# Kernel optimization log

Hardware: AMD Instinct MI355X
Metric: run time of the kernel (lower is better)

Reference implementation:

```python
import jax, jax.numpy as jnp
import numpy as np

K = 4096
D = 128
B = 8
T = 3000
EMA_DECAY = 0.99
EMA_EPS = 1e-05
DEAD_THRESHOLD = 2.0


def setup_inputs() -> dict:
    key = jax.random.key(0)
    k1, k2, k3 = jax.random.split(key, 3)
    z = jax.random.normal(k1, (B, D, T), dtype=jnp.float32)
    codebook = jax.random.normal(k2, (K, D), dtype=jnp.float32) * 0.05  # pretrained-like
    ema_cluster_size = jnp.ones((K,), dtype=jnp.float32)
    ema_embed_avg = codebook.copy()
    return {"z": z, "codebook": codebook,
            "ema_cluster_size": ema_cluster_size, "ema_embed_avg": ema_embed_avg}


def reference(z, codebook, ema_cluster_size, ema_embed_avg):
    b, d, t = z.shape
    z_t = jnp.transpose(z, (0, 2, 1))            # [B, T, D]
    z_flat = z_t.reshape(-1, d)                  # [N, D]

    x2 = jnp.sum(z_flat * z_flat, axis=1, keepdims=True)
    y2 = jnp.sum(codebook * codebook, axis=1)[None, :]
    distances = x2 + y2 - 2.0 * (z_flat @ codebook.T)
    indices = jnp.argmin(distances, axis=1)      # [N]

    q = codebook[indices].reshape(b, t, d)       # [B, T, D]
    loss_commit = jnp.mean((z_t - jax.lax.stop_gradient(q)) ** 2)

    # --- EMA update (torch: @torch.no_grad, training mode) ---
    zf = jax.lax.stop_gradient(z_flat)
    counts = jax.ops.segment_sum(jnp.ones_like(indices, dtype=jnp.float32), indices, num_segments=K)
    embed_sum = jax.ops.segment_sum(zf, indices, num_segments=K)   # [K, D]
    new_cs = ema_cluster_size * EMA_DECAY + counts * (1.0 - EMA_DECAY)
    new_ea = ema_embed_avg * EMA_DECAY + embed_sum * (1.0 - EMA_DECAY)
    n = jnp.sum(new_cs)
    cluster_size = (new_cs + EMA_EPS) / (n + K * EMA_EPS) * n
    embed = new_ea / jnp.clip(cluster_size, 1e-12)[:, None]

    # dead-code reset: resample dead entries from the batch
    dead = new_cs < DEAD_THRESHOLD                                 # [K] bool
    rand_idx = jax.random.randint(jax.random.key(42), (K,), 0, zf.shape[0])
    sampled = zf[rand_idx]                                          # [K, D]
    new_codebook = jnp.where(dead[:, None], sampled, embed)
    new_cs = jnp.where(dead, 1.0, new_cs)
    new_ea = jnp.where(dead[:, None], sampled, new_ea)

    # straight-through estimator
    q_ste = z_t + jax.lax.stop_gradient(q - z_t)
    z_q = jnp.transpose(q_ste, (0, 2, 1))        # [B, D, T]
    codes = indices.reshape(b, t)[None, :, None, :]  # [1, B, 1, T]

    return (z_q, codes, loss_commit, new_codebook, new_cs, new_ea)
```

## Files before the change

kernel.cpp:

```cpp
#include <hip/hip_runtime.h>
#include <stdint.h>

#define KCB 4096
#define DIM 128
#define BSZ 8
#define TLEN 3000
#define NPT 24000
#define KD (KCB*DIM)
#define BDT (BSZ*DIM*TLEN)

#define OFF_ZQ    0
#define OFF_CODES 3072000
#define OFF_LOSS  3096000
#define OFF_CB    3096001
#define OFF_CS    3620289
#define OFF_EA    3624385

#define OUT_ZH    0
#define OUT_ZL    1536000
#define OUT_CBH   3096004
#define OUT_CBL   3358148

#define WS_LOSS   0
#define WS_NTOT   1
#define WS_COUNTS 16
#define WS_Y2     (WS_COUNTS + 4096)
#define WS_X2     (WS_Y2 + 4096)
#define WS_CS0    (WS_X2 + 24000)
#define WS_RAND   (WS_CS0 + 4096)
#define WS_IDX    (WS_RAND + 4096)
#define WS_RCNT   (WS_IDX + 24000)
#define WS_RLIST  (WS_RCNT + 16)
#define RCAP      8192

#define EPS_CAND 2e-3f
#define CAND_MAX 8

typedef __attribute__((ext_vector_type(8))) short bf16x8;
typedef __attribute__((ext_vector_type(4))) float f32x4;
typedef __attribute__((ext_vector_type(4))) int i32x4;

__device__ __forceinline__ unsigned short f2bf(float f) {
  uint32_t u = __float_as_uint(f);
  uint32_t r = (u + 0x7FFFu + ((u >> 16) & 1u)) >> 16;
  return (unsigned short)r;
}
__device__ __forceinline__ float bf2f(unsigned short h) {
  return __uint_as_float(((uint32_t)h) << 16);
}

__device__ __forceinline__ void async16(const void* g, void* l) {
  __builtin_amdgcn_global_load_lds(
      (const __attribute__((address_space(1))) void*)g,
      (__attribute__((address_space(3))) void*)l, 16, 0, 0);
}

__device__ __forceinline__ void threefry2x32(uint32_t k0, uint32_t k1,
                                             uint32_t x0, uint32_t x1,
                                             uint32_t& o0, uint32_t& o1) {
  const uint32_t ks0 = k0, ks1 = k1, ks2 = k0 ^ k1 ^ 0x1BD11BDAu;
  const int r0[4] = {13, 15, 26, 6};
  const int r1[4] = {17, 29, 16, 24};
  x0 += ks0; x1 += ks1;
  #pragma unroll
  for (int i = 0; i < 5; ++i) {
    #pragma unroll
    for (int j = 0; j < 4; ++j) {
      int r = (i & 1) ? r1[j] : r0[j];
      x0 += x1;
      x1 = (x1 << r) | (x1 >> (32 - r));
      x1 ^= x0;
    }
    uint32_t ia = (uint32_t)((i + 1) % 3), ib = (uint32_t)((i + 2) % 3);
    uint32_t a = (ia == 0) ? ks0 : (ia == 1) ? ks1 : ks2;
    uint32_t b = (ib == 0) ? ks0 : (ib == 1) ? ks1 : ks2;
    x0 += a;
    x1 += b + (uint32_t)(i + 1);
  }
  o0 = x0; o1 = x1;
}

__device__ __forceinline__ float np_sumsq_128(const float* __restrict__ v) {
  float r[8];
  #pragma unroll
  for (int j = 0; j < 8; ++j) r[j] = __fmul_rn(v[j], v[j]);
  #pragma unroll
  for (int i = 8; i < DIM; i += 8) {
    #pragma unroll
    for (int j = 0; j < 8; ++j)
      r[j] = __fadd_rn(r[j], __fmul_rn(v[i + j], v[i + j]));
  }
  return __fadd_rn(__fadd_rn(__fadd_rn(r[0], r[1]), __fadd_rn(r[2], r[3])),
                   __fadd_rn(__fadd_rn(r[4], r[5]), __fadd_rn(r[6], r[7])));
}

__global__ void prep_z_kernel(const float* __restrict__ z,
                              unsigned short* __restrict__ zh,
                              unsigned short* __restrict__ zl,
                              float* __restrict__ x2) {
  __shared__ float zt[64 * 132];
  const int tid = threadIdx.x;
  const int n0 = blockIdx.x * 64;
  {
    int nl = tid & 63, dd = tid >> 6;
    int n = n0 + nl;
    int b = n / TLEN, t = n - b * TLEN;
    const float* zbase = z + (size_t)b * (DIM * TLEN) + t;
    #pragma unroll
    for (int d = dd; d < DIM; d += 4) zt[nl * 132 + d] = zbase[(size_t)d * TLEN];
  }
  __syncthreads();
  if (tid < 64) x2[n0 + tid] = np_sumsq_128(zt + tid * 132);

  int r = tid >> 2, d0 = (tid & 3) * 32;
  const float* src = zt + r * 132 + d0;
  size_t base = (size_t)(n0 + r) * 128 + d0;
  #pragma unroll
  for (int c = 0; c < 4; ++c) {
    i32x4 wh, wl;
    #pragma unroll
    for (int q = 0; q < 4; ++q) {
      float f0 = -2.0f * src[c * 8 + q * 2], f1 = -2.0f * src[c * 8 + q * 2 + 1];
      unsigned short h0 = f2bf(f0), h1 = f2bf(f1);
      unsigned short l0 = f2bf(f0 - bf2f(h0)), l1 = f2bf(f1 - bf2f(h1));
      wh[q] = (int)((uint32_t)h0 | ((uint32_t)h1 << 16));
      wl[q] = (int)((uint32_t)l0 | ((uint32_t)l1 << 16));
    }
    *(i32x4*)(zh + base + c * 8) = wh;
    *(i32x4*)(zl + base + c * 8) = wl;
  }
}

__global__ void prep_cb_kernel(const float* __restrict__ cb,
                               unsigned short* __restrict__ cbh,
                               unsigned short* __restrict__ cbl,
                               float* __restrict__ y2) {
  int k = blockIdx.x * 256 + threadIdx.x;
  const float4* row4 = (const float4*)(cb + (size_t)k * DIM);
  float racc[8];
  #pragma unroll
  for (int j = 0; j < 8; ++j) racc[j] = 0.f;
  #pragma unroll 4
  for (int c2 = 0; c2 < 16; ++c2) {
    float4 a = row4[c2 * 2], b = row4[c2 * 2 + 1];
    float f[8] = {a.x, a.y, a.z, a.w, b.x, b.y, b.z, b.w};
    i32x4 wh, wl;
    #pragma unroll
    for (int q = 0; q < 4; ++q) {
      float f0 = f[q * 2], f1 = f[q * 2 + 1];
      unsigned short h0 = f2bf(f0), h1 = f2bf(f1);
      unsigned short l0 = f2bf(f0 - bf2f(h0)), l1 = f2bf(f1 - bf2f(h1));
      wh[q] = (int)((uint32_t)h0 | ((uint32_t)h1 << 16));
      wl[q] = (int)((uint32_t)l0 | ((uint32_t)l1 << 16));
    }
    int cs = c2 ^ (k & 7);
    *(i32x4*)(cbh + (size_t)k * DIM + cs * 8) = wh;
    *(i32x4*)(cbl + (size_t)k * DIM + cs * 8) = wl;
    #pragma unroll
    for (int j = 0; j < 8; ++j)
      racc[j] = __fadd_rn(racc[j], __fmul_rn(f[j], f[j]));
  }
  y2[k] = __fadd_rn(__fadd_rn(__fadd_rn(racc[0], racc[1]), __fadd_rn(racc[2], racc[3])),
                    __fadd_rn(__fadd_rn(racc[4], racc[5]), __fadd_rn(racc[6], racc[7])));
}

__global__ void ea_init_kernel(const float* __restrict__ ema_ea, float* __restrict__ out_ea) {
  int i = blockIdx.x * 256 + threadIdx.x;
  out_ea[i] = 0.99f * ema_ea[i];
}

__launch_bounds__(256)
__global__ void mfma_argmin_kernel(const unsigned short* __restrict__ zh,
                                   const unsigned short* __restrict__ zl,
                                   const unsigned short* __restrict__ cbh,
                                   const unsigned short* __restrict__ cbl,
                                   const float* __restrict__ y2g,
                                   const float* __restrict__ x2g,
                                   const float* __restrict__ z,
                                   const float* __restrict__ cb,
                                   int* __restrict__ idx_out,
                                   float* __restrict__ codes_out,
                                   int* __restrict__ rcnt,
                                   int* __restrict__ rlist) {
  __shared__ alignas(16) unsigned short zh_t[64 * 128];
  __shared__ alignas(16) unsigned short zl_t[64 * 128];
  __shared__ alignas(16) unsigned short Ah_t[64 * 128];
  __shared__ alignas(16) unsigned short Al_t[64 * 128];
  __shared__ float tv[64 * 24];
  __shared__ int   ti[64 * 24];

  const int tid = threadIdx.x;
  const int wv = tid >> 6, lane = tid & 63;
  const int kw = wv & 1, nw = wv >> 1;
  const int lg = lane >> 4, lc = lane & 15;
  const int n0 = blockIdx.x * 64;

  {
    const char* gh = (const char*)cbh + (size_t)(wv * 4) * 1024 + lane * 16;
    const char* gl_ = (const char*)cbl + (size_t)(wv * 4) * 1024 + lane * 16;
    char* lh = (char*)Ah_t + wv * 4096;
    char* ll = (char*)Al_t + wv * 4096;
    #pragma unroll
    for (int i = 0; i < 4; ++i) {
      async16(gh + i * 1024, lh + i * 1024);
      async16(gl_ + i * 1024, ll + i * 1024);
    }
  }

  {
    int r = tid >> 2, c0 = (tid & 3) * 4;
    const i32x4* gzh = (const i32x4*)(zh + (size_t)(n0 + r) * 128);
    const i32x4* gzl = (const i32x4*)(zl + (size_t)(n0 + r) * 128);
    #pragma unroll
    for (int c = 0; c < 4; ++c) {
      int cc = (c0 + c) ^ (r & 7);
      ((i32x4*)zh_t)[r * 16 + cc] = gzh[c0 + c];
      ((i32x4*)zl_t)[r * 16 + cc] = gzl[c0 + c];
    }
  }

  float t1v[2], t2v[2], t3v[2];
  int   t1i[2], t2i[2], t3i[2];
  #pragma unroll
  for (int ns = 0; ns < 2; ++ns) {
    t1v[ns] = t2v[ns] = t3v[ns] = 3.402823466e+38f;
    t1i[ns] = t2i[ns] = t3i[ns] = 0x7FFFFFFF;
  }

  const int arow0 = kw * 32 + lc,  arow1 = kw * 32 + 16 + lc;
  const int zrow0 = nw * 32 + lc,  zrow1 = nw * 32 + 16 + lc;

  for (int tile = 0; tile < 64; ++tile) {
    asm volatile("s_waitcnt vmcnt(0)" ::: "memory");
    __syncthreads();

    const int kb = tile * 64 + kw * 32;
    float4 y40 = *(const float4*)(y2g + kb + lg * 4);
    float4 y41 = *(const float4*)(y2g + kb + 16 + lg * 4);
    f32x4 acc[2][2];
    #pragma unroll
    for (int ns = 0; ns < 2; ++ns) {
      acc[0][ns][0] = y40.x; acc[0][ns][1] = y40.y; acc[0][ns][2] = y40.z; acc[0][ns][3] = y40.w;
      acc[1][ns][0] = y41.x; acc[1][ns][1] = y41.y; acc[1][ns][2] = y41.z; acc[1][ns][3] = y41.w;
    }

    #pragma unroll
    for (int ds = 0; ds < 4; ++ds) {
      int cA0 = (ds * 4 + lg) ^ (arow0 & 7);
      int cA1 = (ds * 4 + lg) ^ (arow1 & 7);
      bf16x8 a0h = *(const bf16x8*)&Ah_t[arow0 * 128 + cA0 * 8];
      bf16x8 a0l = *(const bf16x8*)&Al_t[arow0 * 128 + cA0 * 8];
      bf16x8 a1h = *(const bf16x8*)&Ah_t[arow1 * 128 + cA1 * 8];
      bf16x8 a1l = *(const bf16x8*)&Al_t[arow1 * 128 + cA1 * 8];
      int cz0 = (ds * 4 + lg) ^ (zrow0 & 7);
      int cz1 = (ds * 4 + lg) ^ (zrow1 & 7);
      bf16x8 z0h = *(const bf16x8*)&zh_t[zrow0 * 128 + cz0 * 8];
      bf16x8 z0l = *(const bf16x8*)&zl_t[zrow0 * 128 + cz0 * 8];
      bf16x8 z1h = *(const bf16x8*)&zh_t[zrow1 * 128 + cz1 * 8];
      bf16x8 z1l = *(const bf16x8*)&zl_t[zrow1 * 128 + cz1 * 8];
      acc[0][0] = __builtin_amdgcn_mfma_f32_16x16x32_bf16(a0h, z0h, acc[0][0], 0, 0, 0);
      acc[0][0] = __builtin_amdgcn_mfma_f32_16x16x32_bf16(a0h, z0l, acc[0][0], 0, 0, 0);
      acc[0][0] = __builtin_amdgcn_mfma_f32_16x16x32_bf16(a0l, z0h, acc[0][0], 0, 0, 0);
      acc[0][1] = __builtin_amdgcn_mfma_f32_16x16x32_bf16(a0h, z1h, acc[0][1], 0, 0, 0);
      acc[0][1] = __builtin_amdgcn_mfma_f32_16x16x32_bf16(a0h, z1l, acc[0][1], 0, 0, 0);
      acc[0][1] = __builtin_amdgcn_mfma_f32_16x16x32_bf16(a0l, z1h, acc[0][1], 0, 0, 0);
      acc[1][0] = __builtin_amdgcn_mfma_f32_16x16x32_bf16(a1h, z0h, acc[1][0], 0, 0, 0);
      acc[1][0] = __builtin_amdgcn_mfma_f32_16x16x32_bf16(a1h, z0l, acc[1][0], 0, 0, 0);
      acc[1][0] = __builtin_amdgcn_mfma_f32_16x16x32_bf16(a1l, z0h, acc[1][0], 0, 0, 0);
      acc[1][1] = __builtin_amdgcn_mfma_f32_16x16x32_bf16(a1h, z1h, acc[1][1], 0, 0, 0);
      acc[1][1] = __builtin_amdgcn_mfma_f32_16x16x32_bf16(a1h, z1l, acc[1][1], 0, 0, 0);
      acc[1][1] = __builtin_amdgcn_mfma_f32_16x16x32_bf16(a1l, z1h, acc[1][1], 0, 0, 0);
    }

    __syncthreads();

    if (tile + 1 < 64) {
      const char* gh = (const char*)cbh + (size_t)(tile + 1) * 16384 + (size_t)(wv * 4) * 1024 + lane * 16;
      const char* gl_ = (const char*)cbl + (size_t)(tile + 1) * 16384 + (size_t)(wv * 4) * 1024 + lane * 16;
      char* lh = (char*)Ah_t + wv * 4096;
      char* ll = (char*)Al_t + wv * 4096;
      #pragma unroll
      for (int i = 0; i < 4; ++i) {
        async16(gh + i * 1024, lh + i * 1024);
        async16(gl_ + i * 1024, ll + i * 1024);
      }
    }

    #pragma unroll
    for (int ks = 0; ks < 2; ++ks) {
      int kbase = kb + ks * 16 + lg * 4;
      #pragma unroll
      for (int ns = 0; ns < 2; ++ns) {
        float fm = fminf(fminf(acc[ks][ns][0], acc[ks][ns][1]),
                         fminf(acc[ks][ns][2], acc[ks][ns][3]));
        if (fm < t3v[ns]) {
          #pragma unroll
          for (int q = 0; q < 4; ++q) {
            float v = acc[ks][ns][q];
            int kidx = kbase + q;
            bool c1 = v < t1v[ns], c2 = v < t2v[ns], c3 = v < t3v[ns];
            float n3v = c2 ? t2v[ns] : (c3 ? v : t3v[ns]);
            int   n3i = c2 ? t2i[ns] : (c3 ? kidx : t3i[ns]);
            float n2v = c1 ? t1v[ns] : (c2 ? v : t2v[ns]);
            int   n2i = c1 ? t1i[ns] : (c2 ? kidx : t2i[ns]);
            t1v[ns] = c1 ? v : t1v[ns]; t1i[ns] = c1 ? kidx : t1i[ns];
            t2v[ns] = n2v; t2i[ns] = n2i;
            t3v[ns] = n3v; t3i[ns] = n3i;
          }
        }
      }
    }
  }

  #pragma unroll
  for (int ns = 0; ns < 2; ++ns) {
    int row = nw * 32 + ns * 16 + lc;
    int base = row * 24 + (kw * 4 + lg) * 3;
    tv[base + 0] = t1v[ns]; ti[base + 0] = t1i[ns];
    tv[base + 1] = t2v[ns]; ti[base + 1] = t2i[ns];
    tv[base + 2] = t3v[ns]; ti[base + 2] = t3i[ns];
  }
  __syncthreads();

  if (tid < 64) {
    int n = n0 + tid;
    float bv = 3.402823466e+38f; int bi = 0x7FFFFFFF;
    for (int e = 0; e < 24; ++e) {
      float v = tv[tid * 24 + e]; int i2 = ti[tid * 24 + e];
      if (v < bv || (v == bv && i2 < bi)) { bv = v; bi = i2; }
    }
    int ci[CAND_MAX]; int cnt = 0;
    float lim = bv + EPS_CAND;
    for (int e = 0; e < 24; ++e) {
      float v = tv[tid * 24 + e];
      if (v <= lim && cnt < CAND_MAX) {
        int x = ti[tid * 24 + e];
        int p = cnt++;
        while (p > 0 && ci[p - 1] > x) { ci[p] = ci[p - 1]; --p; }
        ci[p] = x;
      }
    }
    if (cnt == 1) {
      idx_out[n] = ci[0];
      codes_out[n] = (float)ci[0];
    } else {
      int slot = atomicAdd(rcnt, 1);
      if (slot < RCAP) {
        int* e = rlist + slot * 10;
        e[0] = n; e[1] = cnt;
        for (int c = 0; c < CAND_MAX; ++c) e[2 + c] = (c < cnt) ? ci[c] : 0;
        idx_out[n] = ci[0];
        codes_out[n] = (float)ci[0];
      } else {
        int b = n / TLEN, t = n - b * TLEN;
        const float* zr = z + (size_t)b * (DIM * TLEN) + t;
        float bestv = 0.f; int kbest = ci[0];
        for (int c = 0; c < cnt; ++c) {
          int k = ci[c];
          const float* cr = cb + (size_t)k * DIM;
          float dot = 0.f;
          for (int d = 0; d < DIM; ++d)
            dot = __fmaf_rn(zr[(size_t)d * TLEN], cr[d], dot);
          float tt = __fadd_rn(x2g[n], y2g[k]);
          float dist = __fsub_rn(tt, __fmul_rn(2.0f, dot));
          if (c == 0 || dist < bestv) { bestv = dist; kbest = k; }
        }
        idx_out[n] = kbest;
        codes_out[n] = (float)kbest;
      }
    }
  }
}

__global__ void rescore_kernel(const float* __restrict__ z, const float* __restrict__ cb,
                               const float* __restrict__ x2g, const float* __restrict__ y2g,
                               const int* __restrict__ rcnt, const int* __restrict__ rlist,
                               int* __restrict__ idx_out, float* __restrict__ codes_out) {
  int w = (blockIdx.x * 256 + threadIdx.x) >> 6;
  int lane = threadIdx.x & 63;
  int nw = (gridDim.x * 256) >> 6;
  int total = *rcnt; if (total > RCAP) total = RCAP;
  for (int i = w; i < total; i += nw) {
    const int* e = rlist + i * 10;
    int n = e[0], cnt = e[1];
    int b = n / TLEN, t = n - b * TLEN;
    const float* zr = z + (size_t)b * (DIM * TLEN) + t;
    float dist = 3.402823466e+38f;
    int k = e[2 + (lane < cnt ? lane : 0)];
    if (lane < cnt) {
      const float* cr = cb + (size_t)k * DIM;
      float dot = 0.f;
      #pragma unroll 8
      for (int d = 0; d < DIM; ++d)
        dot = __fmaf_rn(zr[(size_t)d * TLEN], cr[d], dot);
      float tt = __fadd_rn(x2g[n], y2g[k]);
      dist = __fsub_rn(tt, __fmul_rn(2.0f, dot));
    }
    float bestv = 0.f; int kbest = 0;
    for (int c = 0; c < cnt; ++c) {
      float v = __shfl(dist, c);
      int kk = __shfl(k, c);
      if (c == 0 || v < bestv) { bestv = v; kbest = kk; }
    }
    if (lane == 0) {
      idx_out[n] = kbest;
      codes_out[n] = (float)kbest;
    }
  }
}

__global__ void ea_scatter_kernel(const unsigned short* __restrict__ zh,
                                  const unsigned short* __restrict__ zl,
                                  const int* __restrict__ idx,
                                  float* __restrict__ ea_out,
                                  float* __restrict__ counts) {
  int n = (blockIdx.x * 256 + threadIdx.x) >> 6;
  int lane = threadIdx.x & 63;
  int k = idx[n];
  uint32_t h = *(const uint32_t*)(zh + (size_t)n * 128 + lane * 2);
  uint32_t l = *(const uint32_t*)(zl + (size_t)n * 128 + lane * 2);
  float f0 = bf2f((unsigned short)(h & 0xffffu)) + bf2f((unsigned short)(l & 0xffffu));
  float f1 = bf2f((unsigned short)(h >> 16)) + bf2f((unsigned short)(l >> 16));
  float* dst = ea_out + (size_t)k * DIM + lane * 2;
  atomicAdd(dst, -0.005f * f0);
  atomicAdd(dst + 1, -0.005f * f1);
  if (lane == 0) atomicAdd(counts + k, 1.0f);
}

__global__ void zq_loss_kernel(const float* __restrict__ z, const float* __restrict__ cb,
                               const int* __restrict__ idx,
                               float* __restrict__ zq_out, float* __restrict__ loss_ws) {
  __shared__ float qt[64 * 132];
  const int tid = threadIdx.x;
  const int n0 = blockIdx.x * 64;
  {
    int r = tid >> 2, c = tid & 3;
    int k = idx[n0 + r];
    const float4* src = (const float4*)(cb + (size_t)k * DIM) + c * 8;
    float4* dst = (float4*)(qt + r * 132) + c * 8;
    #pragma unroll
    for (int j = 0; j < 8; ++j) dst[j] = src[j];
  }
  __syncthreads();
  int nl = tid & 63, dd = tid >> 6;
  int n = n0 + nl;
  int b = n / TLEN, t = n - b * TLEN;
  float* zqb = zq_out + (size_t)b * (DIM * TLEN) + t;
  const float* zb = z + (size_t)b * (DIM * TLEN) + t;
  float sq = 0.f;
  #pragma unroll
  for (int d = dd; d < DIM; d += 4) {
    float q = qt[nl * 132 + d];
    zqb[(size_t)d * TLEN] = q;
    float diff = zb[(size_t)d * TLEN] - q;
    sq = fmaf(diff, diff, sq);
  }
  #pragma unroll
  for (int m = 1; m <= 32; m <<= 1) sq += __shfl_xor(sq, m);
  __shared__ float ps[4];
  if ((tid & 63) == 0) ps[tid >> 6] = sq;
  __syncthreads();
  if (tid == 0) atomicAdd(loss_ws, ps[0] + ps[1] + ps[2] + ps[3]);
}

__global__ void cs_rand_kernel(const float* __restrict__ ema_cs, const float* __restrict__ counts,
                               float* __restrict__ cs0, uint32_t* __restrict__ rnd,
                               float* __restrict__ ntot) {
  int k = blockIdx.x * 256 + threadIdx.x;
  float v = 0.99f * ema_cs[k] + 0.01f * counts[k];
  cs0[k] = v;

  uint32_t o0, o1;
  threefry2x32(0u, 42u, 0u, (uint32_t)k, o0, o1);
  uint32_t bits = o0 ^ o1;
  uint32_t hi = bits >> 16, lo = bits & 0xffffu;
  const uint32_t span = 24000u, mult = 23296u;
  uint32_t off = ((hi % span) * mult + (lo % span)) % span;
  rnd[k] = off;

  float s = v;
  #pragma unroll
  for (int m = 1; m <= 32; m <<= 1) s += __shfl_xor(s, m);
  __shared__ float ps[4];
  if ((threadIdx.x & 63) == 0) ps[threadIdx.x >> 6] = s;
  __syncthreads();
  if (threadIdx.x == 0) atomicAdd(ntot, ps[0] + ps[1] + ps[2] + ps[3]);
}

__global__ void finalize_kernel(const float* __restrict__ z, const float* __restrict__ cs0_ws,
                                const uint32_t* __restrict__ rnd,
                                const float* __restrict__ ntot_ws, const float* __restrict__ loss_ws,
                                float* __restrict__ out) {
  int i = blockIdx.x * 256 + threadIdx.x;
  int k = i >> 7, d = i & (DIM - 1);
  float cs0 = cs0_ws[k];
  float ntot = *ntot_ws;
  float* ea = out + OFF_EA;
  float ea0 = ea[i];
  float csz = (cs0 + 1e-5f) / (ntot + (float)KCB * 1e-5f) * ntot;
  float embed = ea0 / fmaxf(csz, 1e-12f);
  bool dead = cs0 < 2.0f;
  uint32_t rn = rnd[k];
  int bb = (int)(rn / TLEN), tt = (int)(rn % TLEN);
  float sampled = z[(size_t)bb * (DIM * TLEN) + (size_t)d * TLEN + tt];
  out[OFF_CB + i] = dead ? sampled : embed;
  ea[i] = dead ? sampled : ea0;
  if (d == 0) out[OFF_CS + k] = dead ? 1.0f : cs0;
  if (i == 0) out[OFF_LOSS] = (*loss_ws) * (1.0f / (float)BDT);
}

extern "C" void kernel_launch(void* const* d_in, const int* in_sizes, int n_in,
                              void* d_out, int out_size, void* d_ws, size_t ws_size,
                              hipStream_t stream) {
  const float* z      = (const float*)d_in[0];
  const float* cb     = (const float*)d_in[1];
  const float* ema_cs = (const float*)d_in[2];
  const float* ema_ea = (const float*)d_in[3];
  float* out = (float*)d_out;
  float* wsf = (float*)d_ws;

  unsigned short* zh  = (unsigned short*)(out + OUT_ZH);
  unsigned short* zl  = (unsigned short*)(out + OUT_ZL);
  unsigned short* cbh = (unsigned short*)(out + OUT_CBH);
  unsigned short* cbl = (unsigned short*)(out + OUT_CBL);

  hipMemsetAsync(d_ws, 0, (size_t)(16 + 4096) * sizeof(float), stream);
  hipMemsetAsync(wsf + WS_RCNT, 0, 16 * sizeof(float), stream);

  prep_cb_kernel<<<KCB / 256, 256, 0, stream>>>(cb, cbh, cbl, wsf + WS_Y2);
  prep_z_kernel<<<NPT / 64, 256, 0, stream>>>(z, zh, zl, wsf + WS_X2);
  ea_init_kernel<<<KD / 256, 256, 0, stream>>>(ema_ea, out + OFF_EA);

  mfma_argmin_kernel<<<NPT / 64, 256, 0, stream>>>(zh, zl, cbh, cbl,
                                                   wsf + WS_Y2, wsf + WS_X2,
                                                   z, cb,
                                                   (int*)(wsf + WS_IDX), out + OFF_CODES,
                                                   (int*)(wsf + WS_RCNT), (int*)(wsf + WS_RLIST));
  rescore_kernel<<<64, 256, 0, stream>>>(z, cb, wsf + WS_X2, wsf + WS_Y2,
                                         (const int*)(wsf + WS_RCNT), (const int*)(wsf + WS_RLIST),
                                         (int*)(wsf + WS_IDX), out + OFF_CODES);

  ea_scatter_kernel<<<NPT * 64 / 256, 256, 0, stream>>>(zh, zl, (int*)(wsf + WS_IDX),
                                                        out + OFF_EA, wsf + WS_COUNTS);
  zq_loss_kernel<<<NPT / 64, 256, 0, stream>>>(z, cb, (int*)(wsf + WS_IDX),
                                               out + OFF_ZQ, wsf + WS_LOSS);
  cs_rand_kernel<<<KCB / 256, 256, 0, stream>>>(ema_cs, wsf + WS_COUNTS,
                                                wsf + WS_CS0, (uint32_t*)(wsf + WS_RAND),
                                                wsf + WS_NTOT);
  finalize_kernel<<<KD / 256, 256, 0, stream>>>(z, wsf + WS_CS0, (uint32_t*)(wsf + WS_RAND),
                                                wsf + WS_NTOT, wsf + WS_LOSS, out);
}
```

Before: 236.1 us.

## Split codebook search across two block columns with merge kernel

The argmin kernel now splits the codebook into two halves along a second grid dimension. Each block has 128 threads and computes partial best values and indices for 64 points over 2048 codes. Near-ties inside a block are resolved in-kernel with exact FP32 dot products. A new merge kernel picks the winner per point and sends cross-half near-ties to the existing rescore list. This doubles the block count and shrinks shared memory per block to raise occupancy and parallelism, at the cost of an extra kernel launch, partial-result traffic and z tiles loaded twice.

```diff
diff --git a/kernel.cpp b/kernel.cpp
--- a/kernel.cpp
+++ b/kernel.cpp
@@ -32,6 +32,8 @@
 #define WS_RCNT   (WS_IDX + 24000)
 #define WS_RLIST  (WS_RCNT + 16)
 #define RCAP      8192
+#define WS_PBV    (WS_RLIST + RCAP*10)
+#define WS_PBK    (WS_PBV + 2*NPT)
 
 #define EPS_CAND 2e-3f
 #define CAND_MAX 8
@@ -92,6 +94,16 @@
   }
   return __fadd_rn(__fadd_rn(__fadd_rn(r[0], r[1]), __fadd_rn(r[2], r[3])),
                    __fadd_rn(__fadd_rn(r[4], r[5]), __fadd_rn(r[6], r[7])));
+}
+
+__device__ __forceinline__ float np_exact_dist(const float* __restrict__ zr,
+                                               const float* __restrict__ cr,
+                                               float x2v, float y2v) {
+  float dot = 0.f;
+  for (int d = 0; d < DIM; ++d)
+    dot = __fmaf_rn(zr[(size_t)d * TLEN], cr[d], dot);
+  float tt = __fadd_rn(x2v, y2v);
+  return __fsub_rn(tt, __fmul_rn(2.0f, dot));
 }
 
 __global__ void prep_z_kernel(const float* __restrict__ z,
@@ -169,7 +181,7 @@
   out_ea[i] = 0.99f * ema_ea[i];
 }
 
-__launch_bounds__(256)
+__launch_bounds__(128)
 __global__ void mfma_argmin_kernel(const unsigned short* __restrict__ zh,
                                    const unsigned short* __restrict__ zl,
                                    const unsigned short* __restrict__ cbh,
@@ -178,26 +190,24 @@
                                    const float* __restrict__ x2g,
                                    const float* __restrict__ z,
                                    const float* __restrict__ cb,
-                                   int* __restrict__ idx_out,
-                                   float* __restrict__ codes_out,
-                                   int* __restrict__ rcnt,
-                                   int* __restrict__ rlist) {
+                                   float* __restrict__ pbv,
+                                   int* __restrict__ pbk) {
   __shared__ alignas(16) unsigned short zh_t[64 * 128];
   __shared__ alignas(16) unsigned short zl_t[64 * 128];
-  __shared__ alignas(16) unsigned short Ah_t[64 * 128];
-  __shared__ alignas(16) unsigned short Al_t[64 * 128];
-  __shared__ float tv[64 * 24];
-  __shared__ int   ti[64 * 24];
+  __shared__ alignas(16) unsigned short Ah_t[32 * 128];
+  __shared__ alignas(16) unsigned short Al_t[32 * 128];
 
   const int tid = threadIdx.x;
   const int wv = tid >> 6, lane = tid & 63;
-  const int kw = wv & 1, nw = wv >> 1;
+  const int nw = wv;
   const int lg = lane >> 4, lc = lane & 15;
   const int n0 = blockIdx.x * 64;
+  const int hy = blockIdx.y;
+  const size_t kofs = (size_t)hy * 2048;
 
   {
-    const char* gh = (const char*)cbh + (size_t)(wv * 4) * 1024 + lane * 16;
-    const char* gl_ = (const char*)cbl + (size_t)(wv * 4) * 1024 + lane * 16;
+    const char* gh = (const char*)cbh + kofs * 256 + (size_t)wv * 4096 + lane * 16;
+    const char* gl_ = (const char*)cbl + kofs * 256 + (size_t)wv * 4096 + lane * 16;
     char* lh = (char*)Ah_t + wv * 4096;
     char* ll = (char*)Al_t + wv * 4096;
     #pragma unroll
@@ -208,11 +218,11 @@
   }
 
   {
-    int r = tid >> 2, c0 = (tid & 3) * 4;
+    int r = tid >> 1, c0 = (tid & 1) * 8;
     const i32x4* gzh = (const i32x4*)(zh + (size_t)(n0 + r) * 128);
     const i32x4* gzl = (const i32x4*)(zl + (size_t)(n0 + r) * 128);
     #pragma unroll
-    for (int c = 0; c < 4; ++c) {
+    for (int c = 0; c < 8; ++c) {
       int cc = (c0 + c) ^ (r & 7);
       ((i32x4*)zh_t)[r * 16 + cc] = gzh[c0 + c];
       ((i32x4*)zl_t)[r * 16 + cc] = gzl[c0 + c];
@@ -227,14 +237,14 @@
     t1i[ns] = t2i[ns] = t3i[ns] = 0x7FFFFFFF;
   }
 
-  const int arow0 = kw * 32 + lc,  arow1 = kw * 32 + 16 + lc;
-  const int zrow0 = nw * 32 + lc,  zrow1 = nw * 32 + 16 + lc;
-
-  for (int tile = 0; tile < 64; ++tile) {
+  const int arow0 = lc, arow1 = 16 + lc;
+  const int zrow0 = nw * 32 + lc, zrow1 = nw * 32 + 16 + lc;
+
+  for (int st = 0; st < 64; ++st) {
     asm volatile("s_waitcnt vmcnt(0)" ::: "memory");
     __syncthreads();
 
-    const int kb = tile * 64 + kw * 32;
+    const int kb = (int)kofs + st * 32;
     float4 y40 = *(const float4*)(y2g + kb + lg * 4);
     float4 y41 = *(const float4*)(y2g + kb + 16 + lg * 4);
     f32x4 acc[2][2];
@@ -274,9 +284,9 @@
 
     __syncthreads();
 
-    if (tile + 1 < 64) {
-      const char* gh = (const char*)cbh + (size_t)(tile + 1) * 16384 + (size_t)(wv * 4) * 1024 + lane * 16;
-      const char* gl_ = (const char*)cbl + (size_t)(tile + 1) * 16384 + (size_t)(wv * 4) * 1024 + lane * 16;
+    if (st + 1 < 64) {
+      const char* gh = (const char*)cbh + (kofs + (st + 1) * 32) * 256 + (size_t)wv * 4096 + lane * 16;
+      const char* gl_ = (const char*)cbl + (kofs + (st + 1) * 32) * 256 + (size_t)wv * 4096 + lane * 16;
       char* lh = (char*)Ah_t + wv * 4096;
       char* ll = (char*)Al_t + wv * 4096;
       #pragma unroll
@@ -312,10 +322,13 @@
     }
   }
 
+  __syncthreads();
+  float* tv = (float*)Ah_t;
+  int*   ti = (int*)Al_t;
   #pragma unroll
   for (int ns = 0; ns < 2; ++ns) {
     int row = nw * 32 + ns * 16 + lc;
-    int base = row * 24 + (kw * 4 + lg) * 3;
+    int base = row * 12 + lg * 3;
     tv[base + 0] = t1v[ns]; ti[base + 0] = t1i[ns];
     tv[base + 1] = t2v[ns]; ti[base + 1] = t2i[ns];
     tv[base + 2] = t3v[ns]; ti[base + 2] = t3i[ns];
@@ -325,51 +338,58 @@
   if (tid < 64) {
     int n = n0 + tid;
     float bv = 3.402823466e+38f; int bi = 0x7FFFFFFF;
-    for (int e = 0; e < 24; ++e) {
-      float v = tv[tid * 24 + e]; int i2 = ti[tid * 24 + e];
+    for (int e = 0; e < 12; ++e) {
+      float v = tv[tid * 12 + e]; int i2 = ti[tid * 12 + e];
       if (v < bv || (v == bv && i2 < bi)) { bv = v; bi = i2; }
     }
     int ci[CAND_MAX]; int cnt = 0;
     float lim = bv + EPS_CAND;
-    for (int e = 0; e < 24; ++e) {
-      float v = tv[tid * 24 + e];
+    for (int e = 0; e < 12; ++e) {
+      float v = tv[tid * 12 + e];
       if (v <= lim && cnt < CAND_MAX) {
-        int x = ti[tid * 24 + e];
+        int x = ti[tid * 12 + e];
         int p = cnt++;
         while (p > 0 && ci[p - 1] > x) { ci[p] = ci[p - 1]; --p; }
         ci[p] = x;
       }
     }
-    if (cnt == 1) {
-      idx_out[n] = ci[0];
-      codes_out[n] = (float)ci[0];
-    } else {
-      int slot = atomicAdd(rcnt, 1);
-      if (slot < RCAP) {
-        int* e = rlist + slot * 10;
-        e[0] = n; e[1] = cnt;
-        for (int c = 0; c < CAND_MAX; ++c) e[2 + c] = (c < cnt) ? ci[c] : 0;
-        idx_out[n] = ci[0];
-        codes_out[n] = (float)ci[0];
-      } else {
-        int b = n / TLEN, t = n - b * TLEN;
-        const float* zr = z + (size_t)b * (DIM * TLEN) + t;
-        float bestv = 0.f; int kbest = ci[0];
-        for (int c = 0; c < cnt; ++c) {
-          int k = ci[c];
-          const float* cr = cb + (size_t)k * DIM;
-          float dot = 0.f;
-          for (int d = 0; d < DIM; ++d)
-            dot = __fmaf_rn(zr[(size_t)d * TLEN], cr[d], dot);
-          float tt = __fadd_rn(x2g[n], y2g[k]);
-          float dist = __fsub_rn(tt, __fmul_rn(2.0f, dot));
-          if (c == 0 || dist < bestv) { bestv = dist; kbest = k; }
-        }
-        idx_out[n] = kbest;
-        codes_out[n] = (float)kbest;
+    int kbest = ci[0];
+    if (cnt > 1) {
+      int b = n / TLEN, t = n - b * TLEN;
+      const float* zr = z + (size_t)b * (DIM * TLEN) + t;
+      float bestv = 0.f;
+      for (int c = 0; c < cnt; ++c) {
+        float dist = np_exact_dist(zr, cb + (size_t)ci[c] * DIM, x2g[n], y2g[ci[c]]);
+        if (c == 0 || dist < bestv) { bestv = dist; kbest = ci[c]; }
       }
     }
-  }
+    pbv[(size_t)hy * NPT + n] = bv;
+    pbk[(size_t)hy * NPT + n] = kbest;
+  }
+}
+
+__global__ void merge_kernel(const float* __restrict__ pbv, const int* __restrict__ pbk,
+                             int* __restrict__ idx_out, float* __restrict__ codes_out,
+                             int* __restrict__ rcnt, int* __restrict__ rlist) {
+  int n = blockIdx.x * 256 + threadIdx.x;
+  if (n >= NPT) return;
+  float b0 = pbv[n], b1 = pbv[NPT + n];
+  int k0 = pbk[n], k1 = pbk[NPT + n];
+  int w;
+  if (b0 + EPS_CAND < b1) w = k0;
+  else if (b1 + EPS_CAND < b0) w = k1;
+  else {
+    int slot = atomicAdd(rcnt, 1);
+    if (slot < RCAP) {
+      int* e = rlist + slot * 10;
+      e[0] = n; e[1] = 2; e[2] = k0; e[3] = k1;
+      #pragma unroll
+      for (int c = 2; c < CAND_MAX; ++c) e[2 + c] = 0;
+    }
+    w = (b0 <= b1) ? k0 : k1;
+  }
+  idx_out[n] = w;
+  codes_out[n] = (float)w;
 }
 
 __global__ void rescore_kernel(const float* __restrict__ z, const float* __restrict__ cb,
@@ -531,11 +551,14 @@
   prep_z_kernel<<<NPT / 64, 256, 0, stream>>>(z, zh, zl, wsf + WS_X2);
   ea_init_kernel<<<KD / 256, 256, 0, stream>>>(ema_ea, out + OFF_EA);
 
-  mfma_argmin_kernel<<<NPT / 64, 256, 0, stream>>>(zh, zl, cbh, cbl,
-                                                   wsf + WS_Y2, wsf + WS_X2,
-                                                   z, cb,
-                                                   (int*)(wsf + WS_IDX), out + OFF_CODES,
-                                                   (int*)(wsf + WS_RCNT), (int*)(wsf + WS_RLIST));
+  dim3 agrid(NPT / 64, 2);
+  mfma_argmin_kernel<<<agrid, 128, 0, stream>>>(zh, zl, cbh, cbl,
+                                                wsf + WS_Y2, wsf + WS_X2,
+                                                z, cb,
+                                                wsf + WS_PBV, (int*)(wsf + WS_PBK));
+  merge_kernel<<<(NPT + 255) / 256, 256, 0, stream>>>(wsf + WS_PBV, (int*)(wsf + WS_PBK),
+                                                      (int*)(wsf + WS_IDX), out + OFF_CODES,
+                                                      (int*)(wsf + WS_RCNT), (int*)(wsf + WS_RLIST));
   rescore_kernel<<<64, 256, 0, stream>>>(z, cb, wsf + WS_X2, wsf + WS_Y2,
                                          (const int*)(wsf + WS_RCNT), (const int*)(wsf + WS_RLIST),
                                          (int*)(wsf + WS_IDX), out + OFF_CODES);
```

After: 246.6 us. 1.04x slower.
